# Kernel optimization log

Hardware: AMD Instinct MI355X
Metric: run time of the kernel (lower is better)

Reference implementation:

```python
import jax, jax.numpy as jnp
import numpy as np

N = 50000      # nodes
E = 800000     # directed edges (avg degree 16)
F_IN = 128     # input_size
HID = 128      # hidden_size
OUT = 64       # output_size (bottleneck)
EPS = 1e-5     # BatchNorm eps


def setup_inputs() -> dict:
    key = jax.random.key(0)
    ks = jax.random.split(key, 8)
    x = jax.random.normal(ks[0], (N, F_IN), dtype=jnp.float32)
    edge_index = jax.random.randint(ks[1], (2, E), 0, N, dtype=jnp.int64)
    dims = [(F_IN, HID), (HID, HID), (HID, OUT),   # encoder
            (OUT, HID), (HID, HID), (HID, F_IN)]   # decoder
    wkeys = jax.random.split(ks[2], 6)
    inp = {"x": x, "edge_index": edge_index}
    for j, (fi, fo) in enumerate(dims):
        inp[f"W{j}"] = jax.random.normal(wkeys[j], (fi, fo), dtype=jnp.float32) / np.sqrt(fi).astype(np.float32)
        inp[f"b{j}"] = jnp.zeros((fo,), dtype=jnp.float32)
        inp[f"g{j}"] = jnp.ones((fo,), dtype=jnp.float32)   # BN gamma
        inp[f"be{j}"] = jnp.zeros((fo,), dtype=jnp.float32)  # BN beta
    return inp


def _gcn(x, W, b, src, dst, edge_norm, inv_deg):
    # GCNConv: x' = D^-1/2 (A+I) D^-1/2 (x W) + b, sum-aggregation over edges
    h = x @ W                                   # [N, Fo]
    msg = h[src] * edge_norm[:, None]            # [E, Fo] gather + scale
    agg = jax.ops.segment_sum(msg, dst, num_segments=N)  # scatter-add
    agg = agg + h * inv_deg[:, None]             # self-loop term (norm = 1/deg)
    return agg + b


def _bn(x, g, be):
    # BatchNorm1d over nodes, training-mode batch statistics (biased var)
    m = jnp.mean(x, axis=0)
    v = jnp.mean((x - m) ** 2, axis=0)
    return (x - m) * jax.lax.rsqrt(v + EPS) * g + be


def _forward(x, edge_index, Ws, bs, gs, bes):
    src, dst = edge_index[0], edge_index[1]
    # degrees with self-loops (GCN adds self-loops, counts incoming edges)
    deg = jnp.zeros((N,), dtype=x.dtype).at[dst].add(1.0) + 1.0
    dinv_sqrt = jax.lax.rsqrt(deg)
    edge_norm = dinv_sqrt[src] * dinv_sqrt[dst]
    inv_deg = 1.0 / deg
    h = x
    for j in range(6):
        h = _gcn(h, Ws[j], bs[j], src, dst, edge_norm, inv_deg)
        h = _bn(h, gs[j], bes[j])
        if j not in (2, 5):  # ReLU after first two layers of each GNN, not after bn3
            h = jax.nn.relu(h)
    return h


def reference(x, edge_index,
              W0, b0, g0, be0, W1, b1, g1, be1, W2, b2, g2, be2,
              W3, b3, g3, be3, W4, b4, g4, be4, W5, b5, g5, be5):
    Ws = (W0, W1, W2, W3, W4, W5)
    bs = (b0, b1, b2, b3, b4, b5)
    gs = (g0, g1, g2, g3, g4, g5)
    bes = (be0, be1, be2, be3, be4, be5)
    return _forward(x, edge_index, Ws, bs, gs, bes)
```

## Files before the change

### kernel.cpp

```cpp
#include <hip/hip_runtime.h>
#include <hip/hip_bf16.h>
#include <hip/hip_fp16.h>

#define N_NODES 50000
#define N_EDGES 800000
constexpr float BN_EPS = 1e-5f;
constexpr int NCHUNK = (N_NODES + 1023) / 1024;

typedef unsigned short ushortT;
typedef float fx4 __attribute__((ext_vector_type(4)));

__device__ __forceinline__ unsigned short f2bf(float f) {
    __hip_bfloat16 h = __float2bfloat16(f);
    return __builtin_bit_cast(unsigned short, h);
}
__device__ __forceinline__ void cvt4(uint2 v, float* f) {
    f[0] = __uint_as_float(v.x << 16); f[1] = __uint_as_float(v.x & 0xffff0000u);
    f[2] = __uint_as_float(v.y << 16); f[3] = __uint_as_float(v.y & 0xffff0000u);
}
__device__ __forceinline__ float dec_w(unsigned rec) {
    return __half2float(__builtin_bit_cast(__half, (unsigned short)(rec >> 16)));
}


__global__ void count_deg(const int* __restrict__ dst, int* cnts) {
    int e = blockIdx.x * 256 + threadIdx.x;
    if (e < N_EDGES) atomicAdd(&cnts[dst[e]], 1);
}

__global__ void finalize_deg(const int* __restrict__ cnts, float* __restrict__ dinv) {
    int i = blockIdx.x * 256 + threadIdx.x;
    if (i < N_NODES) dinv[i] = rsqrtf((float)cnts[i] + 1.0f);
}

__global__ __launch_bounds__(256)
void scan_block_sums(const int* __restrict__ counts, int* __restrict__ totals) {
    __shared__ int red[4];
    int tid = threadIdx.x;
    int base = blockIdx.x * 1024 + tid * 4;
    int s = 0;
    #pragma unroll
    for (int j = 0; j < 4; ++j) { int i = base + j; if (i < N_NODES) s += counts[i] + 1; }
    #pragma unroll
    for (int d = 1; d < 64; d <<= 1) s += __shfl_xor(s, d, 64);
    if ((tid & 63) == 0) red[tid >> 6] = s;
    __syncthreads();
    if (tid == 0) totals[blockIdx.x] = red[0] + red[1] + red[2] + red[3];
}

__global__ __launch_bounds__(256)
void scan_write(const int* __restrict__ counts, const int* __restrict__ totals,
                int* __restrict__ offs, int* __restrict__ cursor) {
    __shared__ int chunkbase;
    __shared__ int wsum[4];
    int tid = threadIdx.x, lane = tid & 63, wid = tid >> 6;
    if (tid == 0) { int a = 0; for (int i = 0; i < (int)blockIdx.x; ++i) a += totals[i]; chunkbase = a; }
    int base = blockIdx.x * 1024 + tid * 4;
    int v[4]; int s = 0;
    #pragma unroll
    for (int j = 0; j < 4; ++j) { int i = base + j; v[j] = (i < N_NODES) ? counts[i] + 1 : 0; s += v[j]; }
    int ts = s;
    #pragma unroll
    for (int d = 1; d < 64; d <<= 1) { int t = __shfl_up(ts, d, 64); if (lane >= d) ts += t; }
    if (lane == 63) wsum[wid] = ts;
    __syncthreads();
    int wbase = 0;
    #pragma unroll
    for (int w = 0; w < 4; ++w) if (w < wid) wbase += wsum[w];
    int excl = chunkbase + wbase + (ts - s);
    #pragma unroll
    for (int j = 0; j < 4; ++j) {
        int i = base + j;
        if (i < N_NODES) { offs[i] = excl; cursor[i] = excl; }
        excl += v[j];
        if (i == N_NODES - 1) offs[N_NODES] = excl;
    }
}

__global__ void fill_csr(const int* __restrict__ src, const int* __restrict__ dst,
                         const float* __restrict__ dinv, int* cursor,
                         unsigned* __restrict__ edges) {
    int e = blockIdx.x * 256 + threadIdx.x;
    if (e < N_EDGES) {
        int s = src[e], d = dst[e];
        int pos = atomicAdd(&cursor[d], 1);
        unsigned short hb = __builtin_bit_cast(unsigned short, __float2half(dinv[s] * dinv[d]));
        edges[pos] = (unsigned)s | ((unsigned)hb << 16);
    }
}

__global__ void fill_self(const int* __restrict__ counts, const int* __restrict__ offs,
                          unsigned* __restrict__ edges) {
    int i = blockIdx.x * 256 + threadIdx.x;
    if (i < N_NODES) {
        float w = 1.0f / ((float)counts[i] + 1.0f);
        unsigned short hb = __builtin_bit_cast(unsigned short, __float2half(w));
        edges[offs[i] + counts[i]] = (unsigned)i | ((unsigned)hb << 16);
    }
}


template<int FI, int FO, bool BN, bool RELU>
__global__ __launch_bounds__(256)
void gemm_bn(const float* __restrict__ X, const float* __restrict__ W,
             ushortT* __restrict__ Hb, const float* __restrict__ stats_prev,
             const float* __restrict__ g_prev, const float* __restrict__ be_prev) {
    constexpr int CT = FO / 4;
    constexpr int RT = 256 / CT;
    constexpr int ROWS = RT * 4;
    __shared__ ushortT Ws[FI * FO];
    __shared__ float xs[ROWS * FI];
    __shared__ float sscale[FI], sshift[FI];
    if constexpr (BN) {
        if (threadIdx.x < FI) {
            constexpr float invN = 1.0f / (float)N_NODES;
            int k = threadIdx.x;
            float m = stats_prev[k] * invN;
            float var = stats_prev[FI + k] * invN - m * m;
            float is = rsqrtf(var + BN_EPS) * g_prev[k];
            sscale[k] = is;
            sshift[k] = be_prev[k] - m * is;
        }
    }
    for (int i = threadIdx.x * 8; i < FI * FO; i += 256 * 8) {
        float4 w0 = *(const float4*)&W[i];
        float4 w1 = *(const float4*)&W[i + 4];
        ushortT us[8] = { f2bf(w0.x), f2bf(w0.y), f2bf(w0.z), f2bf(w0.w),
                          f2bf(w1.x), f2bf(w1.y), f2bf(w1.z), f2bf(w1.w) };
        *(uint4*)&Ws[i] = *(uint4*)us;
    }
    const int ct = threadIdx.x % CT, rt = threadIdx.x / CT;
    const int col = ct * 4;
    ushortT* Hcol = Hb + (size_t)(col >> 5) * N_NODES * 32 + (col & 31);
    const int ntiles = (N_NODES + ROWS - 1) / ROWS;
    for (int tile = blockIdx.x; tile < ntiles; tile += gridDim.x) {
        const int base = tile * ROWS;
        __syncthreads();
        for (int t = threadIdx.x; t < ROWS * FI / 4; t += 256) {
            int r = t / (FI / 4), k4 = (t % (FI / 4)) * 4;
            int gr = base + r;
            float4 v = (gr < N_NODES) ? *(const float4*)&X[(size_t)gr * FI + k4]
                                      : make_float4(0.f, 0.f, 0.f, 0.f);
            if constexpr (BN) {
                float4 sc = *(const float4*)&sscale[k4];
                float4 sh = *(const float4*)&sshift[k4];
                v.x = fmaf(v.x, sc.x, sh.x); v.y = fmaf(v.y, sc.y, sh.y);
                v.z = fmaf(v.z, sc.z, sh.z); v.w = fmaf(v.w, sc.w, sh.w);
                if constexpr (RELU) {
                    v.x = fmaxf(v.x, 0.f); v.y = fmaxf(v.y, 0.f);
                    v.z = fmaxf(v.z, 0.f); v.w = fmaxf(v.w, 0.f);
                }
            }
            *(float4*)&xs[r * FI + k4] = v;
        }
        __syncthreads();
        float acc[4][4] = {};
        #pragma unroll 2
        for (int k4 = 0; k4 < FI; k4 += 4) {
            float4 xv[4], wv[4];
            #pragma unroll
            for (int ri = 0; ri < 4; ++ri)
                xv[ri] = *(const float4*)&xs[(rt * 4 + ri) * FI + k4];
            #pragma unroll
            for (int j = 0; j < 4; ++j) {
                ushort4 wu = *(const ushort4*)&Ws[(k4 + j) * FO + col];
                wv[j] = make_float4(__uint_as_float((unsigned)wu.x << 16),
                                    __uint_as_float((unsigned)wu.y << 16),
                                    __uint_as_float((unsigned)wu.z << 16),
                                    __uint_as_float((unsigned)wu.w << 16));
            }
            #pragma unroll
            for (int ri = 0; ri < 4; ++ri) {
                #pragma unroll
                for (int j = 0; j < 4; ++j) {
                    float xk = ((const float*)&xv[ri])[j];
                    acc[ri][0] = fmaf(xk, wv[j].x, acc[ri][0]);
                    acc[ri][1] = fmaf(xk, wv[j].y, acc[ri][1]);
                    acc[ri][2] = fmaf(xk, wv[j].z, acc[ri][2]);
                    acc[ri][3] = fmaf(xk, wv[j].w, acc[ri][3]);
                }
            }
        }
        #pragma unroll
        for (int ri = 0; ri < 4; ++ri) {
            int row = base + rt * 4 + ri;
            if (row < N_NODES) {
                ushortT us[4] = { f2bf(acc[ri][0]), f2bf(acc[ri][1]),
                                  f2bf(acc[ri][2]), f2bf(acc[ri][3]) };
                *(ushort4*)&Hcol[(size_t)row * 32] = *(ushort4*)us;
            }
        }
    }
}


template<int FO>
__global__ __launch_bounds__(256)
void aggregate_sliced(const ushortT* __restrict__ Hb, const int* __restrict__ offs,
                      const unsigned* __restrict__ edges, const float* __restrict__ bias,
                      float* __restrict__ out, float* __restrict__ stats) {
    constexpr int NPASS = FO / 32;
    constexpr int XPP = 8 / NPASS;
    constexpr int RPX = N_NODES / XPP;
    const int b = blockIdx.x;
    const int b7 = b & 7;
    const int pass = b7 / XPP;
    const int rx = b7 % XPP;
    const int o = b >> 3;
    const int NB = gridDim.x >> 3;
    const int r_lo = rx * RPX;
    const int r_hi = r_lo + RPX;
    const int lt = threadIdx.x & 7;
    const int sub = threadIdx.x >> 3;
    const uint2* S2 = (const uint2*)(Hb + (size_t)pass * N_NODES * 32);
    const int f0 = pass * 32 + lt * 4;
    const float4 b4 = *(const float4*)&bias[f0];
    float s[4] = {}, s2[4] = {};
    for (int r = r_lo + o * 32 + sub; r < r_hi; r += NB * 32) {
        float a[4] = { b4.x, b4.y, b4.z, b4.w };
        int e = offs[r], en = offs[r + 1];
        for (; e + 2 <= en; e += 2) {
            uint2 ee = *(const uint2*)&edges[e];
            uint2 v0 = S2[(size_t)(ee.x & 0xffff) * 8 + lt];
            uint2 v1 = S2[(size_t)(ee.y & 0xffff) * 8 + lt];
            float w0 = dec_w(ee.x), w1 = dec_w(ee.y);
            float g0[4], g1[4];
            cvt4(v0, g0); cvt4(v1, g1);
            #pragma unroll
            for (int j = 0; j < 4; ++j) a[j] = fmaf(g0[j], w0, a[j]);
            #pragma unroll
            for (int j = 0; j < 4; ++j) a[j] = fmaf(g1[j], w1, a[j]);
        }
        if (e < en) {
            unsigned ee = edges[e];
            float w = dec_w(ee);
            float g[4];
            cvt4(S2[(size_t)(ee & 0xffff) * 8 + lt], g);
            #pragma unroll
            for (int j = 0; j < 4; ++j) a[j] = fmaf(g[j], w, a[j]);
        }
        fx4 o4 = { a[0], a[1], a[2], a[3] };
        __builtin_nontemporal_store(o4, (fx4*)&out[(size_t)r * FO + f0]);
        #pragma unroll
        for (int j = 0; j < 4; ++j) { s[j] += a[j]; s2[j] += a[j] * a[j]; }
    }
    __shared__ float ls[256][4], ls2[256][4];
    #pragma unroll
    for (int j = 0; j < 4; ++j) { ls[threadIdx.x][j] = s[j]; ls2[threadIdx.x][j] = s2[j]; }
    __syncthreads();
    if (sub == 0) {
        for (int t = 1; t < 32; ++t) {
            #pragma unroll
            for (int j = 0; j < 4; ++j) {
                s[j] += ls[t * 8 + lt][j];
                s2[j] += ls2[t * 8 + lt][j];
            }
        }
        #pragma unroll
        for (int j = 0; j < 4; ++j) {
            atomicAdd(&stats[f0 + j], s[j]);
            atomicAdd(&stats[FO + f0 + j], s2[j]);
        }
    }
}


template<int FO, bool RELU>
__global__ __launch_bounds__(256)
void bn_norm(const float* __restrict__ X, const float* __restrict__ stats,
             const float* __restrict__ g, const float* __restrict__ be,
             float* __restrict__ Y) {
    constexpr float invN = 1.0f / (float)N_NODES;
    const int total4 = N_NODES * FO / 4;
    for (int idx = blockIdx.x * 256 + threadIdx.x; idx < total4; idx += gridDim.x * 256) {
        int o4 = (idx * 4) & (FO - 1);
        float4 x = ((const float4*)X)[idx];
        float y[4];
        #pragma unroll
        for (int j = 0; j < 4; ++j) {
            int o = o4 + j;
            float m = stats[o] * invN;
            float v = stats[FO + o] * invN - m * m;
            float istd = rsqrtf(v + BN_EPS);
            float val = ((&x.x)[j] - m) * istd * g[o] + be[o];
            if (RELU) val = fmaxf(val, 0.f);
            y[j] = val;
        }
        ((float4*)Y)[idx] = make_float4(y[0], y[1], y[2], y[3]);
    }
}


extern "C" void kernel_launch(void* const* d_in, const int* in_sizes, int n_in,
                              void* d_out, int out_size, void* d_ws, size_t ws_size,
                              hipStream_t stream) {
    const float* x  = (const float*)d_in[0];
    const int* ei   = (const int*)d_in[1];
    const int* src  = ei;
    const int* dst  = ei + N_EDGES;

    size_t off = 0;
    auto alloc = [&](size_t bytes) -> void* {
        void* p = (char*)d_ws + off;
        off += (bytes + 255) & ~(size_t)255;
        return p;
    };
    int*      counts = (int*)     alloc((size_t)N_NODES * 4);
    int*      offs   = (int*)     alloc((size_t)(N_NODES + 1) * 4);
    int*      cursor = (int*)     alloc((size_t)N_NODES * 4);
    int*      totals = (int*)     alloc((size_t)NCHUNK * 4);
    float*    dinv   = (float*)   alloc((size_t)N_NODES * 4);
    unsigned* edges  = (unsigned*)alloc((size_t)(N_EDGES + N_NODES) * 4);
    float*    stats  = (float*)   alloc(6 * 256 * 4);
    ushortT*  Hb     = (ushortT*) alloc((size_t)N_NODES * 128 * 2);
    float*    A0     = (float*)   alloc((size_t)N_NODES * 128 * 4);
    float*    A1     = (float*)   alloc((size_t)N_NODES * 128 * 4);

    (void)hipMemsetAsync(counts, 0, (size_t)N_NODES * 4, stream);
    (void)hipMemsetAsync(stats, 0, 6 * 256 * 4, stream);

    count_deg<<<(N_EDGES + 255) / 256, 256, 0, stream>>>(dst, counts);
    finalize_deg<<<(N_NODES + 255) / 256, 256, 0, stream>>>(counts, dinv);
    scan_block_sums<<<NCHUNK, 256, 0, stream>>>(counts, totals);
    scan_write<<<NCHUNK, 256, 0, stream>>>(counts, totals, offs, cursor);
    fill_csr<<<(N_EDGES + 255) / 256, 256, 0, stream>>>(src, dst, dinv, cursor, edges);
    fill_self<<<(N_NODES + 255) / 256, 256, 0, stream>>>(counts, offs, edges);

    const float* W[6]; const float* b[6]; const float* g[6]; const float* be[6];
    for (int j = 0; j < 6; ++j) {
        W[j]  = (const float*)d_in[2 + 4 * j];
        b[j]  = (const float*)d_in[3 + 4 * j];
        g[j]  = (const float*)d_in[4 + 4 * j];
        be[j] = (const float*)d_in[5 + 4 * j];
    }
    float* st[6];
    for (int j = 0; j < 6; ++j) st[j] = stats + j * 256;
    float* dout = (float*)d_out;

    gemm_bn<128, 128, false, false><<<768, 256, 0, stream>>>(x, W[0], Hb, nullptr, nullptr, nullptr);
    aggregate_sliced<128><<<2048, 256, 0, stream>>>(Hb, offs, edges, b[0], A0, st[0]);

    gemm_bn<128, 128, true, true><<<768, 256, 0, stream>>>(A0, W[1], Hb, st[0], g[0], be[0]);
    aggregate_sliced<128><<<2048, 256, 0, stream>>>(Hb, offs, edges, b[1], A1, st[1]);

    gemm_bn<128, 64, true, true><<<768, 256, 0, stream>>>(A1, W[2], Hb, st[1], g[1], be[1]);
    aggregate_sliced<64><<<2048, 256, 0, stream>>>(Hb, offs, edges, b[2], A0, st[2]);

    gemm_bn<64, 128, true, false><<<768, 256, 0, stream>>>(A0, W[3], Hb, st[2], g[2], be[2]);
    aggregate_sliced<128><<<2048, 256, 0, stream>>>(Hb, offs, edges, b[3], A1, st[3]);

    gemm_bn<128, 128, true, true><<<768, 256, 0, stream>>>(A1, W[4], Hb, st[3], g[3], be[3]);
    aggregate_sliced<128><<<2048, 256, 0, stream>>>(Hb, offs, edges, b[4], A0, st[4]);

    gemm_bn<128, 128, true, true><<<768, 256, 0, stream>>>(A0, W[5], Hb, st[4], g[4], be[4]);
    aggregate_sliced<128><<<2048, 256, 0, stream>>>(Hb, offs, edges, b[5], dout, st[5]);
    bn_norm<128, false><<<2048, 256, 0, stream>>>(dout, st[5], g[5], be[5], dout);
}
```

Baseline: 929.3 us.

## Pin aggregation feature slices to XCC and balance rows with atomic work queue

The aggregation kernel now reads the hardware XCC id and uses it to pick which 32-feature slice a block handles, instead of inferring it from blockIdx modulo 8. Rows are no longer split statically: each block grabs batches of 128 rows from a per-slice atomic cursor until all nodes are done. The aim is to keep each slice's gathered feature table resident in one XCC's L2 and to even out degree-driven load imbalance. The cost is an atomic plus two block barriers per batch and extra cursor state that must be zeroed each call. Correctness relies on every XCC receiving blocks so that every slice is covered.

```diff
diff --git a/kernel.cpp b/kernel.cpp
--- a/kernel.cpp
+++ b/kernel.cpp
@@ -198,51 +198,56 @@
 __global__ __launch_bounds__(256)
 void aggregate_sliced(const ushortT* __restrict__ Hb, const int* __restrict__ offs,
                       const unsigned* __restrict__ edges, const float* __restrict__ bias,
-                      float* __restrict__ out, float* __restrict__ stats) {
+                      float* __restrict__ out, float* __restrict__ stats,
+                      int* __restrict__ cursor) {
     constexpr int NPASS = FO / 32;
-    constexpr int XPP = 8 / NPASS;
-    constexpr int RPX = N_NODES / XPP;
-    const int b = blockIdx.x;
-    const int b7 = b & 7;
-    const int pass = b7 / XPP;
-    const int rx = b7 % XPP;
-    const int o = b >> 3;
-    const int NB = gridDim.x >> 3;
-    const int r_lo = rx * RPX;
-    const int r_hi = r_lo + RPX;
+    int xcc;
+    asm("s_getreg_b32 %0, hwreg(HW_REG_XCC_ID)" : "=s"(xcc));
+    const int pass = xcc & (NPASS - 1);
     const int lt = threadIdx.x & 7;
     const int sub = threadIdx.x >> 3;
     const uint2* S2 = (const uint2*)(Hb + (size_t)pass * N_NODES * 32);
     const int f0 = pass * 32 + lt * 4;
     const float4 b4 = *(const float4*)&bias[f0];
     float s[4] = {}, s2[4] = {};
-    for (int r = r_lo + o * 32 + sub; r < r_hi; r += NB * 32) {
-        float a[4] = { b4.x, b4.y, b4.z, b4.w };
-        int e = offs[r], en = offs[r + 1];
-        for (; e + 2 <= en; e += 2) {
-            uint2 ee = *(const uint2*)&edges[e];
-            uint2 v0 = S2[(size_t)(ee.x & 0xffff) * 8 + lt];
-            uint2 v1 = S2[(size_t)(ee.y & 0xffff) * 8 + lt];
-            float w0 = dec_w(ee.x), w1 = dec_w(ee.y);
-            float g0[4], g1[4];
-            cvt4(v0, g0); cvt4(v1, g1);
-            #pragma unroll
-            for (int j = 0; j < 4; ++j) a[j] = fmaf(g0[j], w0, a[j]);
-            #pragma unroll
-            for (int j = 0; j < 4; ++j) a[j] = fmaf(g1[j], w1, a[j]);
-        }
-        if (e < en) {
-            unsigned ee = edges[e];
-            float w = dec_w(ee);
-            float g[4];
-            cvt4(S2[(size_t)(ee & 0xffff) * 8 + lt], g);
-            #pragma unroll
-            for (int j = 0; j < 4; ++j) a[j] = fmaf(g[j], w, a[j]);
-        }
-        fx4 o4 = { a[0], a[1], a[2], a[3] };
-        __builtin_nontemporal_store(o4, (fx4*)&out[(size_t)r * FO + f0]);
+    __shared__ int batch_s;
+    for (;;) {
+        __syncthreads();
+        if (threadIdx.x == 0) batch_s = atomicAdd(cursor + pass, 128);
+        __syncthreads();
+        const int batch = batch_s;
+        if (batch >= N_NODES) break;
         #pragma unroll
-        for (int j = 0; j < 4; ++j) { s[j] += a[j]; s2[j] += a[j] * a[j]; }
+        for (int it = 0; it < 4; ++it) {
+            int r = batch + it * 32 + sub;
+            if (r >= N_NODES) break;
+            float a[4] = { b4.x, b4.y, b4.z, b4.w };
+            int e = offs[r], en = offs[r + 1];
+            for (; e + 2 <= en; e += 2) {
+                uint2 ee = *(const uint2*)&edges[e];
+                uint2 v0 = S2[(size_t)(ee.x & 0xffff) * 8 + lt];
+                uint2 v1 = S2[(size_t)(ee.y & 0xffff) * 8 + lt];
+                float w0 = dec_w(ee.x), w1 = dec_w(ee.y);
+                float g0[4], g1[4];
+                cvt4(v0, g0); cvt4(v1, g1);
+                #pragma unroll
+                for (int j = 0; j < 4; ++j) a[j] = fmaf(g0[j], w0, a[j]);
+                #pragma unroll
+                for (int j = 0; j < 4; ++j) a[j] = fmaf(g1[j], w1, a[j]);
+            }
+            if (e < en) {
+                unsigned ee = edges[e];
+                float w = dec_w(ee);
+                float g[4];
+                cvt4(S2[(size_t)(ee & 0xffff) * 8 + lt], g);
+                #pragma unroll
+                for (int j = 0; j < 4; ++j) a[j] = fmaf(g[j], w, a[j]);
+            }
+            fx4 o4 = { a[0], a[1], a[2], a[3] };
+            __builtin_nontemporal_store(o4, (fx4*)&out[(size_t)r * FO + f0]);
+            #pragma unroll
+            for (int j = 0; j < 4; ++j) { s[j] += a[j]; s2[j] += a[j] * a[j]; }
+        }
     }
     __shared__ float ls[256][4], ls2[256][4];
     #pragma unroll
@@ -312,12 +317,14 @@
     float*    dinv   = (float*)   alloc((size_t)N_NODES * 4);
     unsigned* edges  = (unsigned*)alloc((size_t)(N_EDGES + N_NODES) * 4);
     float*    stats  = (float*)   alloc(6 * 256 * 4);
+    int*      wcurs  = (int*)     alloc(64 * 4);
     ushortT*  Hb     = (ushortT*) alloc((size_t)N_NODES * 128 * 2);
     float*    A0     = (float*)   alloc((size_t)N_NODES * 128 * 4);
     float*    A1     = (float*)   alloc((size_t)N_NODES * 128 * 4);
 
     (void)hipMemsetAsync(counts, 0, (size_t)N_NODES * 4, stream);
     (void)hipMemsetAsync(stats, 0, 6 * 256 * 4, stream);
+    (void)hipMemsetAsync(wcurs, 0, 64 * 4, stream);
 
     count_deg<<<(N_EDGES + 255) / 256, 256, 0, stream>>>(dst, counts);
     finalize_deg<<<(N_NODES + 255) / 256, 256, 0, stream>>>(counts, dinv);
@@ -338,21 +345,21 @@
     float* dout = (float*)d_out;
 
     gemm_bn<128, 128, false, false><<<768, 256, 0, stream>>>(x, W[0], Hb, nullptr, nullptr, nullptr);
-    aggregate_sliced<128><<<2048, 256, 0, stream>>>(Hb, offs, edges, b[0], A0, st[0]);
+    aggregate_sliced<128><<<2048, 256, 0, stream>>>(Hb, offs, edges, b[0], A0, st[0], wcurs + 0);
 
     gemm_bn<128, 128, true, true><<<768, 256, 0, stream>>>(A0, W[1], Hb, st[0], g[0], be[0]);
-    aggregate_sliced<128><<<2048, 256, 0, stream>>>(Hb, offs, edges, b[1], A1, st[1]);
+    aggregate_sliced<128><<<2048, 256, 0, stream>>>(Hb, offs, edges, b[1], A1, st[1], wcurs + 8);
 
     gemm_bn<128, 64, true, true><<<768, 256, 0, stream>>>(A1, W[2], Hb, st[1], g[1], be[1]);
-    aggregate_sliced<64><<<2048, 256, 0, stream>>>(Hb, offs, edges, b[2], A0, st[2]);
+    aggregate_sliced<64><<<2048, 256, 0, stream>>>(Hb, offs, edges, b[2], A0, st[2], wcurs + 16);
 
     gemm_bn<64, 128, true, false><<<768, 256, 0, stream>>>(A0, W[3], Hb, st[2], g[2], be[2]);
-    aggregate_sliced<128><<<2048, 256, 0, stream>>>(Hb, offs, edges, b[3], A1, st[3]);
+    aggregate_sliced<128><<<2048, 256, 0, stream>>>(Hb, offs, edges, b[3], A1, st[3], wcurs + 24);
 
     gemm_bn<128, 128, true, true><<<768, 256, 0, stream>>>(A1, W[4], Hb, st[3], g[3], be[3]);
-    aggregate_sliced<128><<<2048, 256, 0, stream>>>(Hb, offs, edges, b[4], A0, st[4]);
+    aggregate_sliced<128><<<2048, 256, 0, stream>>>(Hb, offs, edges, b[4], A0, st[4], wcurs + 32);
 
     gemm_bn<128, 128, true, true><<<768, 256, 0, stream>>>(A0, W[5], Hb, st[4], g[4], be[4]);
-    aggregate_sliced<128><<<2048, 256, 0, stream>>>(Hb, offs, edges, b[5], dout, st[5]);
+    aggregate_sliced<128><<<2048, 256, 0, stream>>>(Hb, offs, edges, b[5], dout, st[5], wcurs + 40);
     bn_norm<128, false><<<2048, 256, 0, stream>>>(dout, st[5], g[5], be[5], dout);
 }
```

After: 1.010 ms. +8.6%, slower.

## Replace scalar FMA GEMM with MFMA bf16 matrix-core GEMM per 64-row tile

Applied to the files above, without the earlier changes.

Rewrites the per-layer dense transform to use 16x16x32 bf16 MFMA instructions. Each wave handles 16 rows, and A fragments are loaded straight from global memory with BN and ReLU folded in before the bf16 conversion. Weights are stored transposed in LDS with padding, and the grid launches one block per 64-row tile instead of a persistent loop. The intent is to cut the FMA-bound GEMM time, at the cost of scalar 2-byte output stores and re-staging the weights in every block.

```diff
diff --git a/kernel.cpp b/kernel.cpp
--- a/kernel.cpp
+++ b/kernel.cpp
@@ -6,9 +6,11 @@
 #define N_EDGES 800000
 constexpr float BN_EPS = 1e-5f;
 constexpr int NCHUNK = (N_NODES + 1023) / 1024;
+constexpr int NTILES = (N_NODES + 63) / 64;
 
 typedef unsigned short ushortT;
 typedef float fx4 __attribute__((ext_vector_type(4)));
+typedef short bf16x8 __attribute__((ext_vector_type(8)));
 
 __device__ __forceinline__ unsigned short f2bf(float f) {
     __hip_bfloat16 h = __float2bfloat16(f);
@@ -102,93 +104,75 @@
 
 template<int FI, int FO, bool BN, bool RELU>
 __global__ __launch_bounds__(256)
-void gemm_bn(const float* __restrict__ X, const float* __restrict__ W,
-             ushortT* __restrict__ Hb, const float* __restrict__ stats_prev,
-             const float* __restrict__ g_prev, const float* __restrict__ be_prev) {
-    constexpr int CT = FO / 4;
-    constexpr int RT = 256 / CT;
-    constexpr int ROWS = RT * 4;
-    __shared__ ushortT Ws[FI * FO];
-    __shared__ float xs[ROWS * FI];
+void gemm_mfma(const float* __restrict__ X, const float* __restrict__ W,
+               ushortT* __restrict__ Hb, const float* __restrict__ stats_prev,
+               const float* __restrict__ g_prev, const float* __restrict__ be_prev) {
+    constexpr int KS = FI / 32;
+    constexpr int CT = FO / 16;
+    constexpr int LDW = FI + 8;
+    __shared__ ushortT Wt[FO * LDW];
     __shared__ float sscale[FI], sshift[FI];
+    const int tid = threadIdx.x;
     if constexpr (BN) {
-        if (threadIdx.x < FI) {
+        if (tid < FI) {
             constexpr float invN = 1.0f / (float)N_NODES;
-            int k = threadIdx.x;
-            float m = stats_prev[k] * invN;
-            float var = stats_prev[FI + k] * invN - m * m;
-            float is = rsqrtf(var + BN_EPS) * g_prev[k];
-            sscale[k] = is;
-            sshift[k] = be_prev[k] - m * is;
-        }
-    }
-    for (int i = threadIdx.x * 8; i < FI * FO; i += 256 * 8) {
-        float4 w0 = *(const float4*)&W[i];
-        float4 w1 = *(const float4*)&W[i + 4];
-        ushortT us[8] = { f2bf(w0.x), f2bf(w0.y), f2bf(w0.z), f2bf(w0.w),
-                          f2bf(w1.x), f2bf(w1.y), f2bf(w1.z), f2bf(w1.w) };
-        *(uint4*)&Ws[i] = *(uint4*)us;
-    }
-    const int ct = threadIdx.x % CT, rt = threadIdx.x / CT;
-    const int col = ct * 4;
-    ushortT* Hcol = Hb + (size_t)(col >> 5) * N_NODES * 32 + (col & 31);
-    const int ntiles = (N_NODES + ROWS - 1) / ROWS;
-    for (int tile = blockIdx.x; tile < ntiles; tile += gridDim.x) {
-        const int base = tile * ROWS;
-        __syncthreads();
-        for (int t = threadIdx.x; t < ROWS * FI / 4; t += 256) {
-            int r = t / (FI / 4), k4 = (t % (FI / 4)) * 4;
-            int gr = base + r;
-            float4 v = (gr < N_NODES) ? *(const float4*)&X[(size_t)gr * FI + k4]
-                                      : make_float4(0.f, 0.f, 0.f, 0.f);
-            if constexpr (BN) {
-                float4 sc = *(const float4*)&sscale[k4];
-                float4 sh = *(const float4*)&sshift[k4];
-                v.x = fmaf(v.x, sc.x, sh.x); v.y = fmaf(v.y, sc.y, sh.y);
-                v.z = fmaf(v.z, sc.z, sh.z); v.w = fmaf(v.w, sc.w, sh.w);
-                if constexpr (RELU) {
-                    v.x = fmaxf(v.x, 0.f); v.y = fmaxf(v.y, 0.f);
-                    v.z = fmaxf(v.z, 0.f); v.w = fmaxf(v.w, 0.f);
-                }
+            float m = stats_prev[tid] * invN;
+            float var = stats_prev[FI + tid] * invN - m * m;
+            float is = rsqrtf(var + BN_EPS) * g_prev[tid];
+            sscale[tid] = is;
+            sshift[tid] = be_prev[tid] - m * is;
+        }
+    }
+    for (int i = tid; i < FI * FO; i += 256) {
+        int k = i / FO, n = i % FO;
+        Wt[n * LDW + k] = f2bf(W[i]);
+    }
+    __syncthreads();
+
+    const int wid = tid >> 6, lane = tid & 63;
+    const int lm = lane & 15, lg = lane >> 4;
+    const int rbase = blockIdx.x * 64 + wid * 16;
+
+    const int arow = rbase + lm;
+    const float* xr = X + (size_t)(arow < N_NODES ? arow : 0) * FI;
+
+    fx4 acc[CT] = {};
+    #pragma unroll
+    for (int ks = 0; ks < KS; ++ks) {
+        const int k0 = ks * 32 + lg * 8;
+        float xv[8];
+        *(float4*)&xv[0] = *(const float4*)&xr[k0];
+        *(float4*)&xv[4] = *(const float4*)&xr[k0 + 4];
+        if constexpr (BN) {
+            float sc[8], sh[8];
+            *(float4*)&sc[0] = *(const float4*)&sscale[k0];
+            *(float4*)&sc[4] = *(const float4*)&sscale[k0 + 4];
+            *(float4*)&sh[0] = *(const float4*)&sshift[k0];
+            *(float4*)&sh[4] = *(const float4*)&sshift[k0 + 4];
+            #pragma unroll
+            for (int j = 0; j < 8; ++j) {
+                xv[j] = fmaf(xv[j], sc[j], sh[j]);
+                if constexpr (RELU) xv[j] = fmaxf(xv[j], 0.f);
             }
-            *(float4*)&xs[r * FI + k4] = v;
-        }
-        __syncthreads();
-        float acc[4][4] = {};
-        #pragma unroll 2
-        for (int k4 = 0; k4 < FI; k4 += 4) {
-            float4 xv[4], wv[4];
-            #pragma unroll
-            for (int ri = 0; ri < 4; ++ri)
-                xv[ri] = *(const float4*)&xs[(rt * 4 + ri) * FI + k4];
-            #pragma unroll
-            for (int j = 0; j < 4; ++j) {
-                ushort4 wu = *(const ushort4*)&Ws[(k4 + j) * FO + col];
-                wv[j] = make_float4(__uint_as_float((unsigned)wu.x << 16),
-                                    __uint_as_float((unsigned)wu.y << 16),
-                                    __uint_as_float((unsigned)wu.z << 16),
-                                    __uint_as_float((unsigned)wu.w << 16));
-            }
-            #pragma unroll
-            for (int ri = 0; ri < 4; ++ri) {
-                #pragma unroll
-                for (int j = 0; j < 4; ++j) {
-                    float xk = ((const float*)&xv[ri])[j];
-                    acc[ri][0] = fmaf(xk, wv[j].x, acc[ri][0]);
-                    acc[ri][1] = fmaf(xk, wv[j].y, acc[ri][1]);
-                    acc[ri][2] = fmaf(xk, wv[j].z, acc[ri][2]);
-                    acc[ri][3] = fmaf(xk, wv[j].w, acc[ri][3]);
-                }
-            }
-        }
-        #pragma unroll
-        for (int ri = 0; ri < 4; ++ri) {
-            int row = base + rt * 4 + ri;
-            if (row < N_NODES) {
-                ushortT us[4] = { f2bf(acc[ri][0]), f2bf(acc[ri][1]),
-                                  f2bf(acc[ri][2]), f2bf(acc[ri][3]) };
-                *(ushort4*)&Hcol[(size_t)row * 32] = *(ushort4*)us;
-            }
+        }
+        short us[8];
+        #pragma unroll
+        for (int j = 0; j < 8; ++j) us[j] = (short)f2bf(xv[j]);
+        bf16x8 afrag = *(const bf16x8*)us;
+        #pragma unroll
+        for (int ct = 0; ct < CT; ++ct) {
+            bf16x8 bfrag = *(const bf16x8*)&Wt[(ct * 16 + lm) * LDW + k0];
+            acc[ct] = __builtin_amdgcn_mfma_f32_16x16x32_bf16(afrag, bfrag, acc[ct], 0, 0, 0);
+        }
+    }
+    #pragma unroll
+    for (int ct = 0; ct < CT; ++ct) {
+        int col = ct * 16 + lm;
+        ushortT* hp = Hb + (size_t)(col >> 5) * N_NODES * 32 + (col & 31);
+        #pragma unroll
+        for (int j = 0; j < 4; ++j) {
+            int r = rbase + lg * 4 + j;
+            if (r < N_NODES) hp[(size_t)r * 32] = f2bf(acc[ct][j]);
         }
     }
 }
@@ -337,22 +321,22 @@
     for (int j = 0; j < 6; ++j) st[j] = stats + j * 256;
     float* dout = (float*)d_out;
 
-    gemm_bn<128, 128, false, false><<<768, 256, 0, stream>>>(x, W[0], Hb, nullptr, nullptr, nullptr);
+    gemm_mfma<128, 128, false, false><<<NTILES, 256, 0, stream>>>(x, W[0], Hb, nullptr, nullptr, nullptr);
     aggregate_sliced<128><<<2048, 256, 0, stream>>>(Hb, offs, edges, b[0], A0, st[0]);
 
-    gemm_bn<128, 128, true, true><<<768, 256, 0, stream>>>(A0, W[1], Hb, st[0], g[0], be[0]);
+    gemm_mfma<128, 128, true, true><<<NTILES, 256, 0, stream>>>(A0, W[1], Hb, st[0], g[0], be[0]);
     aggregate_sliced<128><<<2048, 256, 0, stream>>>(Hb, offs, edges, b[1], A1, st[1]);
 
-    gemm_bn<128, 64, true, true><<<768, 256, 0, stream>>>(A1, W[2], Hb, st[1], g[1], be[1]);
+    gemm_mfma<128, 64, true, true><<<NTILES, 256, 0, stream>>>(A1, W[2], Hb, st[1], g[1], be[1]);
     aggregate_sliced<64><<<2048, 256, 0, stream>>>(Hb, offs, edges, b[2], A0, st[2]);
 
-    gemm_bn<64, 128, true, false><<<768, 256, 0, stream>>>(A0, W[3], Hb, st[2], g[2], be[2]);
+    gemm_mfma<64, 128, true, false><<<NTILES, 256, 0, stream>>>(A0, W[3], Hb, st[2], g[2], be[2]);
     aggregate_sliced<128><<<2048, 256, 0, stream>>>(Hb, offs, edges, b[3], A1, st[3]);
 
-    gemm_bn<128, 128, true, true><<<768, 256, 0, stream>>>(A1, W[4], Hb, st[3], g[3], be[3]);
+    gemm_mfma<128, 128, true, true><<<NTILES, 256, 0, stream>>>(A1, W[4], Hb, st[3], g[3], be[3]);
     aggregate_sliced<128><<<2048, 256, 0, stream>>>(Hb, offs, edges, b[4], A0, st[4]);
 
-    gemm_bn<128, 128, true, true><<<768, 256, 0, stream>>>(A0, W[5], Hb, st[4], g[4], be[4]);
+    gemm_mfma<128, 128, true, true><<<NTILES, 256, 0, stream>>>(A0, W[5], Hb, st[4], g[4], be[4]);
     aggregate_sliced<128><<<2048, 256, 0, stream>>>(Hb, offs, edges, b[5], dout, st[5]);
     bn_norm<128, false><<<2048, 256, 0, stream>>>(dout, st[5], g[5], be[5], dout);
 }
```

After: 834.0 us. 1.11x faster.
